# Optimization experiments

Measured on AMD Instinct MI355X. Metric: run time of the kernel, lower is better.

The kernel has to match this reference:

```python
import jax, jax.numpy as jnp
import numpy as np

B, L = 32, 100
NQ = 500
S = NQ + 1          # n_question + 1 skills
DK, DA, DE = 64, 64, 128
NE, NAT, NIT = 20000, 3000, 3000


def _xavier(k, shape):
    fan_out, fan_in = shape[0], shape[1]
    bound = float(np.sqrt(6.0 / (fan_in + fan_out)))
    return jax.random.uniform(k, shape, jnp.float32, -bound, bound)


def setup_inputs() -> dict:
    key = jax.random.key(0)
    ks = jax.random.split(key, 24)
    inp = {
        'e_data': jax.random.randint(ks[0], (B, L), 0, NE),
        'a_data': jax.random.randint(ks[1], (B, L), 0, 2, dtype=jnp.int32),
        'at_data': jax.random.randint(ks[2], (B, L), 0, NAT),
        'it_data': jax.random.randint(ks[3], (B, L), 0, NIT),
        'q_matrix': (jax.random.uniform(ks[4], (NE + 10, S)) < 0.05).astype(jnp.float32),
        'h0': _xavier(ks[5], (S, DK)),
        'e_embed': _xavier(ks[6], (NE + 10, DE)),
        'at_embed': _xavier(ks[7], (NAT + 10, DK)),
        'it_embed': _xavier(ks[8], (NIT + 10, DK)),
        'W1': _xavier(ks[9], (DK, DA + DE + DK)), 'b1': jnp.zeros((DK,)),
        'W2': _xavier(ks[10], (DK, 4 * DK)),      'b2': jnp.zeros((DK,)),
        'W3': _xavier(ks[11], (DK, 4 * DK)),      'b3': jnp.zeros((DK,)),
        'W4': _xavier(ks[12], (DK, 3 * DK)),      'b4': jnp.zeros((DK,)),
        'W5': _xavier(ks[13], (DK, DE + DK)),     'b5': jnp.zeros((DK,)),
    }
    return inp


def reference(e_data, a_data, at_data, it_data, q_matrix, h0, e_embed,
              at_embed, it_embed, W1, b1, W2, b2, W3, b3, W4, b4, W5, b5):
    b, l = e_data.shape
    dk = h0.shape[1]
    e_emb = e_embed[e_data]            # (B,L,DE)
    it_emb = it_embed[it_data]         # (B,L,DK)
    at_emb = at_embed[at_data]         # (B,L,DK)
    a_rep = jnp.broadcast_to(a_data.astype(jnp.float32)[:, :, None], (b, l, DA))
    # linear_1 over concat(e, at, a): all learning vectors, computed once
    all_learning = jnp.concatenate([e_emb, at_emb, a_rep], axis=2) @ W1.T + b1  # (B,L,DK)

    h_pre0 = jnp.broadcast_to(h0[None], (b,) + h0.shape)      # (B,S,DK)
    h_tilde0 = q_matrix[e_data[:, 0]] @ h0                    # (B,DK)
    learning0 = jnp.zeros((b, dk), jnp.float32)

    xs = dict(
        e_t=e_data[:, :-1].T,                                  # (L-1,B)
        it_t=jnp.swapaxes(it_emb[:, :-1], 0, 1),               # (L-1,B,DK)
        learn_t=jnp.swapaxes(all_learning[:, :-1], 0, 1),      # (L-1,B,DK)
        e_next=e_data[:, 1:].T,                                # (L-1,B)
        e_emb_next=jnp.swapaxes(e_emb[:, 1:], 0, 1),           # (L-1,B,DE)
    )

    def step(carry, x):
        h_pre, h_tilde_pre, learning_pre = carry
        q_e = q_matrix[x['e_t']]                               # (B,S)
        g_in = jnp.concatenate([learning_pre, x['it_t'], x['learn_t'], h_tilde_pre], 1)
        learning_gain = jnp.tanh(g_in @ W2.T + b2)
        gamma_l = jax.nn.sigmoid(g_in @ W3.T + b3)
        LG = gamma_l * (learning_gain + 1.0) * 0.5             # (B,DK)
        LG_tilde = q_e[:, :, None] * LG[:, None, :]            # (B,S,DK)
        s = h_pre.shape[1]
        f_in = jnp.concatenate([
            h_pre,
            jnp.broadcast_to(LG[:, None, :], (b, s, dk)),
            jnp.broadcast_to(x['it_t'][:, None, :], (b, s, dk)),
        ], axis=2)
        gamma_f = jax.nn.sigmoid(f_in @ W4.T + b4)             # (B,S,DK)
        h = LG_tilde + gamma_f * h_pre
        q_next = q_matrix[x['e_next']]                         # (B,S)
        h_tilde = jnp.einsum('bs,bsd->bd', q_next, h)
        y = jax.nn.sigmoid(jnp.concatenate([x['e_emb_next'], h_tilde], 1) @ W5.T + b5).sum(1) / dk
        return (h, h_tilde, x['learn_t']), y

    _, ys = jax.lax.scan(step, (h_pre0, h_tilde0, learning0), xs)
    pred = jnp.concatenate([jnp.zeros((b, 1), jnp.float32), ys.T], axis=1)  # (B,L)
    return pred
```

## Files before the change

kernel.cpp:

```cpp
#include <hip/hip_runtime.h>
#include <hip/hip_bf16.h>

namespace {

constexpr int B  = 32;
constexpr int L  = 100;
constexpr int S  = 501;
constexpr int DK = 64;
constexpr int DE = 128;

typedef __attribute__((ext_vector_type(8))) short short8v;
typedef __attribute__((ext_vector_type(4))) float f32x4;
typedef unsigned int u32;

__device__ __forceinline__ float sigm(float x) {
    return __fdividef(1.0f, 1.0f + __expf(-x));
}
__device__ __forceinline__ unsigned short f2bf(float f) {
    u32 u = __float_as_uint(f);
    u += 0x7FFFu + ((u >> 16) & 1u);
    return (unsigned short)(u >> 16);
}
__device__ __forceinline__ u32 pack2(float a, float b) {
    return (u32)f2bf(a) | ((u32)f2bf(b) << 16);
}

__global__ __launch_bounds__(256) void k_init(
    const float* __restrict__ W1, const float* __restrict__ W2,
    const float* __restrict__ W3, const float* __restrict__ W4,
    const float* __restrict__ W5,
    float* __restrict__ W1T, float* __restrict__ W2T, float* __restrict__ W3T,
    float* __restrict__ W4T, float* __restrict__ W5T,
    float* __restrict__ pred)
{
    const int idx = blockIdx.x * 256 + threadIdx.x;
    const int st  = gridDim.x * 256;
    for (int i = idx; i < 64 * 256; i += st) {
        int dd = i >> 8, kk = i & 255;
        W1T[kk * 64 + dd] = W1[i];
        W2T[kk * 64 + dd] = W2[i];
        W3T[kk * 64 + dd] = W3[i];
    }
    for (int i = idx; i < 64 * 192; i += st) {
        int dd = i / 192, kk = i % 192;
        W4T[kk * 64 + dd] = W4[i];
        W5T[kk * 64 + dd] = W5[i];
    }
    if (idx < B) pred[idx * L] = 0.0f;
}

__global__ __launch_bounds__(256) void k_all_learning(
    const int* __restrict__ e_data, const int* __restrict__ a_data,
    const int* __restrict__ at_data,
    const float* __restrict__ e_embed, const float* __restrict__ at_embed,
    const float* __restrict__ W1T, const float* __restrict__ b1,
    float* __restrict__ allL)
{
    __shared__ float in_s[4][257];
    const int g = threadIdx.x >> 6;
    const int d = threadIdx.x & 63;
    const int row = blockIdx.x * 4 + g;
    const int e  = e_data[row];
    const int at = at_data[row];
    in_s[g][d]       = e_embed[(size_t)e * DE + d];
    in_s[g][64 + d]  = e_embed[(size_t)e * DE + 64 + d];
    in_s[g][128 + d] = at_embed[(size_t)at * DK + d];
    in_s[g][192 + d] = (float)a_data[row];
    __syncthreads();
    float acc = b1[d];
    #pragma unroll 8
    for (int k = 0; k < 256; ++k) acc += W1T[k * 64 + d] * in_s[g][k];
    allL[row * DK + d] = acc;
}

__global__ __launch_bounds__(256) void k_pre(
    const int* __restrict__ e_data, const int* __restrict__ it_data,
    const float* __restrict__ e_embed, const float* __restrict__ it_embed,
    const float* __restrict__ allL,
    const float* __restrict__ W2T, const float* __restrict__ W3T,
    const float* __restrict__ W4T, const float* __restrict__ W5T,
    const float* __restrict__ b2, const float* __restrict__ b3,
    const float* __restrict__ b4, const float* __restrict__ b5,
    float* __restrict__ G2, float* __restrict__ G3,
    float* __restrict__ G4it, float* __restrict__ prey)
{
    __shared__ float lp[4][64], its[4][64], ln[4][64], ee[4][128];
    const int g = threadIdx.x >> 6;
    const int d = threadIdx.x & 63;
    const int row = blockIdx.x * 4 + g;
    const int t = row % L;
    lp[g][d]  = (t == 0) ? 0.0f : allL[(row - 1) * 64 + d];
    its[g][d] = it_embed[(size_t)it_data[row] * 64 + d];
    ln[g][d]  = allL[row * 64 + d];
    const int e = e_data[row];
    ee[g][d]      = e_embed[(size_t)e * DE + d];
    ee[g][64 + d] = e_embed[(size_t)e * DE + 64 + d];
    __syncthreads();
    float g2 = b2[d], g3 = b3[d], g4 = b4[d], py = b5[d];
    #pragma unroll 4
    for (int k = 0; k < 64; ++k) {
        const float l0 = lp[g][k], i0 = its[g][k], n0 = ln[g][k];
        g2 += W2T[k * 64 + d] * l0 + W2T[(64 + k) * 64 + d] * i0 + W2T[(128 + k) * 64 + d] * n0;
        g3 += W3T[k * 64 + d] * l0 + W3T[(64 + k) * 64 + d] * i0 + W3T[(128 + k) * 64 + d] * n0;
        g4 += W4T[(128 + k) * 64 + d] * i0;
        py += W5T[k * 64 + d] * ee[g][k] + W5T[(64 + k) * 64 + d] * ee[g][64 + k];
    }
    G2[row * 64 + d]   = g2;
    G3[row * 64 + d]   = g3;
    G4it[row * 64 + d] = g4;
    prey[row * 64 + d] = py;
}

__global__ __launch_bounds__(512, 1) void k_steps(
    const float* __restrict__ G2, const float* __restrict__ G3,
    const float* __restrict__ G4it,
    const float* __restrict__ W2, const float* __restrict__ W3,
    const float* __restrict__ W4,
    const float* __restrict__ q_matrix, const int* __restrict__ e_data,
    const float* __restrict__ h0, float* __restrict__ hthist)
{
    __shared__ unsigned short hB[512 * 72];
    __shared__ float2 qP[512];
    __shared__ float htH[100 * 64];
    __shared__ float htS[64], LGs[64], Vs[64];
    __shared__ float red[512], red2[512];
    __shared__ float red4[32 * 64];
    __shared__ int eRow[104];

    const int tid = threadIdx.x;
    const int b   = blockIdx.x;
    const int l   = tid & 63;
    const int w   = tid >> 6;
    const int lm  = l & 15;
    const int lk  = l >> 4;
    const int d   = tid & 63;
    const int kg  = tid >> 6;

    float w2r[8], w3r[8], wbr[8];
    #pragma unroll
    for (int j = 0; j < 8; ++j) {
        w2r[j] = W2[d * 256 + 192 + kg * 8 + j];
        w3r[j] = W3[d * 256 + 192 + kg * 8 + j];
        wbr[j] = W4[d * 192 + 64  + kg * 8 + j];
    }

    short8v afr[4][2];
    #pragma unroll
    for (int dt = 0; dt < 4; ++dt)
        #pragma unroll
        for (int kc = 0; kc < 2; ++kc) {
            const float* src = W4 + (size_t)(dt * 16 + lm) * 192 + kc * 32 + lk * 8;
            union { unsigned short us[8]; short8v v; } u;
            #pragma unroll
            for (int j = 0; j < 8; ++j) u.us[j] = f2bf(src[j]);
            afr[dt][kc] = u.v;
        }

    if (tid < L) eRow[tid] = e_data[b * L + tid];

    f32x4 hreg[4][4];
    #pragma unroll
    for (int st = 0; st < 4; ++st) {
        const int s = (w * 4 + st) * 16 + lm;
        #pragma unroll
        for (int dt = 0; dt < 4; ++dt) {
            const int d0 = dt * 16 + lk * 4;
            f32x4 hv = {0.f, 0.f, 0.f, 0.f};
            if (s < S) hv = *(const f32x4*)(h0 + (size_t)s * 64 + d0);
            hreg[st][dt] = hv;
            *(uint2*)&hB[s * 72 + d0] =
                make_uint2(pack2(hv.x, hv.y), pack2(hv.z, hv.w));
        }
    }
    __syncthreads();

    {
        const float q0 = (tid < S) ? q_matrix[(size_t)eRow[0] * S + tid] : 0.f;
        const float q1 = (tid < S) ? q_matrix[(size_t)eRow[1] * S + tid] : 0.f;
        qP[tid] = make_float2(q0, q1);
    }
    float g2v = 0.f, g3v = 0.f, g4v = 0.f;
    if (tid < 64) {
        g2v = G2[(b * L) * 64 + l];
        g3v = G3[(b * L) * 64 + l];
        g4v = G4it[(b * L) * 64 + l];
    }
    __syncthreads();

    {
        f32x4 part[4];
        #pragma unroll
        for (int dt = 0; dt < 4; ++dt) part[dt] = f32x4{0.f, 0.f, 0.f, 0.f};
        #pragma unroll
        for (int st = 0; st < 4; ++st) {
            const int s = (w * 4 + st) * 16 + lm;
            const float qe = qP[s].x;
            #pragma unroll
            for (int dt = 0; dt < 4; ++dt) part[dt] += qe * hreg[st][dt];
        }
        #pragma unroll
        for (int dt = 0; dt < 4; ++dt)
            #pragma unroll
            for (int i = 0; i < 4; ++i) {
                float v = part[dt][i];
                v += __shfl_xor(v, 1); v += __shfl_xor(v, 2);
                part[dt][i] = v;
            }
        if ((lm & 3) == 0) {
            const int g = w * 4 + (lm >> 2);
            #pragma unroll
            for (int dt = 0; dt < 4; ++dt)
                *(f32x4*)&red4[g * 64 + dt * 16 + lk * 4] = part[dt];
        }
    }
    __syncthreads();
    if (tid < 64) {
        float htd = 0.f;
        #pragma unroll
        for (int g = 0; g < 32; ++g) htd += red4[g * 64 + l];
        htS[l] = htd;
        htH[l] = htd;
    }
    __syncthreads();

    float qn_reg = 0.f;

    for (int t = 0; t < L - 1; ++t) {
        if (t > 0) {
            const float2 qold = qP[tid];
            qP[tid] = make_float2(qold.y, qn_reg);
        }
        {
            const int tn = (t + 2 < L) ? t + 2 : L - 1;
            qn_reg = (tid < S) ? q_matrix[(size_t)eRow[tn] * S + tid] : 0.f;
        }
        short8v bfr[4][2];
        #pragma unroll
        for (int st = 0; st < 4; ++st) {
            const int s = (w * 4 + st) * 16 + lm;
            #pragma unroll
            for (int kc = 0; kc < 2; ++kc)
                bfr[st][kc] = *(const short8v*)&hB[s * 72 + kc * 32 + lk * 8];
        }
        {
            const f32x4 h4a = *(const f32x4*)&htS[kg * 8];
            const f32x4 h4b = *(const f32x4*)&htS[kg * 8 + 4];
            float p2 = 0.f, p3 = 0.f;
            #pragma unroll
            for (int j = 0; j < 4; ++j) {
                p2 += w2r[j] * h4a[j] + w2r[4 + j] * h4b[j];
                p3 += w3r[j] * h4a[j] + w3r[4 + j] * h4b[j];
            }
            red[kg * 64 + d]  = p2;
            red2[kg * 64 + d] = p3;
        }
        __syncthreads();

        if (tid < 64) {
            float g2 = g2v, g3 = g3v;
            #pragma unroll
            for (int ww = 0; ww < 8; ++ww) { g2 += red[ww * 64 + d]; g3 += red2[ww * 64 + d]; }
            LGs[d] = sigm(g3) * (tanhf(g2) + 1.0f) * 0.5f;
        }
        __syncthreads();

        {
            const f32x4 l4a = *(const f32x4*)&LGs[kg * 8];
            const f32x4 l4b = *(const f32x4*)&LGs[kg * 8 + 4];
            float pv = 0.f;
            #pragma unroll
            for (int j = 0; j < 4; ++j)
                pv += wbr[j] * l4a[j] + wbr[4 + j] * l4b[j];
            red[kg * 64 + d] = pv;
        }
        __syncthreads();

        if (tid < 64) {
            float v = g4v;
            #pragma unroll
            for (int ww = 0; ww < 8; ++ww) v += red[ww * 64 + d];
            Vs[d] = v;
            g2v = G2[(b * L + t + 1) * 64 + l];
            g3v = G3[(b * L + t + 1) * 64 + l];
            g4v = G4it[(b * L + t + 1) * 64 + l];
        }
        __syncthreads();

        float2 qv[4];
        #pragma unroll
        for (int st = 0; st < 4; ++st) qv[st] = qP[(w * 4 + st) * 16 + lm];

        f32x4 part[4];
        #pragma unroll
        for (int dt = 0; dt < 4; ++dt) part[dt] = f32x4{0.f, 0.f, 0.f, 0.f};

        #pragma unroll
        for (int half = 0; half < 2; ++half) {
            f32x4 acc[2][4];
            #pragma unroll
            for (int d2 = 0; d2 < 2; ++d2)
                #pragma unroll
                for (int st = 0; st < 4; ++st) acc[d2][st] = f32x4{0.f, 0.f, 0.f, 0.f};

            #pragma unroll
            for (int d2 = 0; d2 < 2; ++d2) {
                const int dt = half * 2 + d2;
                #pragma unroll
                for (int st = 0; st < 4; ++st) {
                    acc[d2][st] = __builtin_amdgcn_mfma_f32_16x16x32_bf16(
                        afr[dt][0], bfr[st][0], acc[d2][st], 0, 0, 0);
                    acc[d2][st] = __builtin_amdgcn_mfma_f32_16x16x32_bf16(
                        afr[dt][1], bfr[st][1], acc[d2][st], 0, 0, 0);
                }
            }

            #pragma unroll
            for (int d2 = 0; d2 < 2; ++d2) {
                const int dt = half * 2 + d2;
                const int d0 = dt * 16 + lk * 4;
                const f32x4 lg4 = *(const f32x4*)&LGs[d0];
                const f32x4 v4  = *(const f32x4*)&Vs[d0];
                #pragma unroll
                for (int st = 0; st < 4; ++st) {
                    const int s = (w * 4 + st) * 16 + lm;
                    const float qe = qv[st].x;
                    const float qq = qv[st].y;
                    const f32x4 a  = acc[d2][st];
                    const f32x4 ho = hreg[st][dt];
                    f32x4 hn;
                    hn.x = qe * lg4.x + sigm(a.x + v4.x) * ho.x;
                    hn.y = qe * lg4.y + sigm(a.y + v4.y) * ho.y;
                    hn.z = qe * lg4.z + sigm(a.z + v4.z) * ho.z;
                    hn.w = qe * lg4.w + sigm(a.w + v4.w) * ho.w;
                    hreg[st][dt] = hn;
                    *(uint2*)&hB[s * 72 + d0] =
                        make_uint2(pack2(hn.x, hn.y), pack2(hn.z, hn.w));
                    part[dt] += qq * hn;
                }
            }
        }

        #pragma unroll
        for (int dt = 0; dt < 4; ++dt)
            #pragma unroll
            for (int i = 0; i < 4; ++i) {
                float v = part[dt][i];
                v += __shfl_xor(v, 1); v += __shfl_xor(v, 2);
                part[dt][i] = v;
            }
        if ((lm & 3) == 0) {
            const int g = w * 4 + (lm >> 2);
            #pragma unroll
            for (int dt = 0; dt < 4; ++dt)
                *(f32x4*)&red4[g * 64 + dt * 16 + lk * 4] = part[dt];
        }
        __syncthreads();

        if (tid < 64) {
            float htd = 0.f;
            #pragma unroll
            for (int g = 0; g < 32; ++g) htd += red4[g * 64 + l];
            htS[l] = htd;
            htH[(t + 1) * 64 + l] = htd;
        }
        __syncthreads();
    }

    for (int i = tid; i < 100 * 64; i += 512)
        hthist[(size_t)(i >> 6) * (B * 64) + b * 64 + (i & 63)] = htH[i];
}

__global__ __launch_bounds__(64) void k_y(
    const float* __restrict__ hthist, const float* __restrict__ prey,
    const float* __restrict__ W5T, float* __restrict__ pred)
{
    __shared__ float HT[64];
    const int j = blockIdx.x + 1;
    const int b = blockIdx.y;
    const int d = threadIdx.x;
    HT[d] = hthist[(size_t)j * (B * 64) + b * 64 + d];
    __syncthreads();
    float acc = prey[(b * L + j) * 64 + d];
    #pragma unroll 8
    for (int k = 0; k < 64; ++k) acc += W5T[(128 + k) * 64 + d] * HT[k];
    float y = sigm(acc);
    #pragma unroll
    for (int m = 1; m < 64; m <<= 1) y += __shfl_xor(y, m);
    if (d == 0) pred[b * L + j] = y * (1.0f / 64.0f);
}

}

extern "C" void kernel_launch(void* const* d_in, const int* in_sizes, int n_in,
                              void* d_out, int out_size, void* d_ws, size_t ws_size,
                              hipStream_t stream)
{
    const int*   e_data   = (const int*)d_in[0];
    const int*   a_data   = (const int*)d_in[1];
    const int*   at_data  = (const int*)d_in[2];
    const int*   it_data  = (const int*)d_in[3];
    const float* q_matrix = (const float*)d_in[4];
    const float* h0       = (const float*)d_in[5];
    const float* e_embed  = (const float*)d_in[6];
    const float* at_embed = (const float*)d_in[7];
    const float* it_embed = (const float*)d_in[8];
    const float* W1 = (const float*)d_in[9];  const float* b1 = (const float*)d_in[10];
    const float* W2 = (const float*)d_in[11]; const float* b2 = (const float*)d_in[12];
    const float* W3 = (const float*)d_in[13]; const float* b3 = (const float*)d_in[14];
    const float* W4 = (const float*)d_in[15]; const float* b4 = (const float*)d_in[16];
    const float* W5 = (const float*)d_in[17]; const float* b5 = (const float*)d_in[18];
    float* pred = (float*)d_out;

    float* ws   = (float*)d_ws;
    float* W1T    = ws;
    float* W2T    = W1T    + 16384;
    float* W3T    = W2T    + 16384;
    float* W4T    = W3T    + 16384;
    float* W5T    = W4T    + 12288;
    float* allL   = W5T    + 12288;
    float* G2     = allL   + 204800;
    float* G3     = G2     + 204800;
    float* G4it   = G3     + 204800;
    float* prey   = G4it   + 204800;
    float* hthist = prey   + 204800;

    hipLaunchKernelGGL(k_init, dim3(64), dim3(256), 0, stream,
                       W1, W2, W3, W4, W5, W1T, W2T, W3T, W4T, W5T, pred);
    hipLaunchKernelGGL(k_all_learning, dim3(B * L / 4), dim3(256), 0, stream,
                       e_data, a_data, at_data, e_embed, at_embed, W1T, b1, allL);
    hipLaunchKernelGGL(k_pre, dim3(B * L / 4), dim3(256), 0, stream,
                       e_data, it_data, e_embed, it_embed, allL,
                       W2T, W3T, W4T, W5T, b2, b3, b4, b5, G2, G3, G4it, prey);
    hipLaunchKernelGGL(k_steps, dim3(B), dim3(512), 0, stream,
                       G2, G3, G4it, W2, W3, W4, q_matrix, e_data, h0, hthist);
    hipLaunchKernelGGL(k_y, dim3(L - 1, B), dim3(64), 0, stream,
                       hthist, prey, W5T, pred);
}
```

Before: 755.1 us.

## Move forget-gate MFMA off the critical path and pad reduction buffer

The per-step h_pre·W4 MFMA product depends only on the previous h, so it is now computed right after h is updated and stored, rather than after the gate-vector reduction and barrier of the next step. This lets the matrix work overlap with the small vector phase, at the cost of keeping a full 4x4 accumulator array in registers across iterations. The red4 reduction buffer is padded to a stride of 68 to reduce LDS bank conflicts, and the ht reduction is moved to the loop head. pack2 now rounds to bf16 by adding half an ulp instead of round-to-nearest-even, which saves a few integer ops per value but changes tie rounding slightly.

Result: faster. 726.4 us (median of 2 runs) (-3.8%).

```diff
diff --git a/kernel.cpp b/kernel.cpp
--- a/kernel.cpp
+++ b/kernel.cpp
@@ -22,7 +22,9 @@
     return (unsigned short)(u >> 16);
 }
 __device__ __forceinline__ u32 pack2(float a, float b) {
-    return (u32)f2bf(a) | ((u32)f2bf(b) << 16);
+    const u32 ua = __float_as_uint(a) + 0x8000u;
+    const u32 ub = __float_as_uint(b) + 0x8000u;
+    return (ua >> 16) | (ub & 0xFFFF0000u);
 }
 
 __global__ __launch_bounds__(256) void k_init(
@@ -124,7 +126,7 @@
     __shared__ float htH[100 * 64];
     __shared__ float htS[64], LGs[64], Vs[64];
     __shared__ float red[512], red2[512];
-    __shared__ float red4[32 * 64];
+    __shared__ float red4[32 * 68];
     __shared__ int eRow[104];
 
     const int tid = threadIdx.x;
@@ -172,6 +174,27 @@
                 make_uint2(pack2(hv.x, hv.y), pack2(hv.z, hv.w));
         }
     }
+
+    f32x4 acc[4][4];
+    {
+        short8v bfr[4][2];
+        #pragma unroll
+        for (int st = 0; st < 4; ++st) {
+            const int s = (w * 4 + st) * 16 + lm;
+            #pragma unroll
+            for (int kc = 0; kc < 2; ++kc)
+                bfr[st][kc] = *(const short8v*)&hB[s * 72 + kc * 32 + lk * 8];
+        }
+        #pragma unroll
+        for (int dt = 0; dt < 4; ++dt)
+            #pragma unroll
+            for (int st = 0; st < 4; ++st) {
+                f32x4 z = {0.f, 0.f, 0.f, 0.f};
+                z = __builtin_amdgcn_mfma_f32_16x16x32_bf16(afr[dt][0], bfr[st][0], z, 0, 0, 0);
+                z = __builtin_amdgcn_mfma_f32_16x16x32_bf16(afr[dt][1], bfr[st][1], z, 0, 0, 0);
+                acc[dt][st] = z;
+            }
+    }
     __syncthreads();
 
     {
@@ -210,22 +233,23 @@
             const int g = w * 4 + (lm >> 2);
             #pragma unroll
             for (int dt = 0; dt < 4; ++dt)
-                *(f32x4*)&red4[g * 64 + dt * 16 + lk * 4] = part[dt];
-        }
-    }
-    __syncthreads();
-    if (tid < 64) {
-        float htd = 0.f;
-        #pragma unroll
-        for (int g = 0; g < 32; ++g) htd += red4[g * 64 + l];
-        htS[l] = htd;
-        htH[l] = htd;
+                *(f32x4*)&red4[g * 68 + dt * 16 + lk * 4] = part[dt];
+        }
     }
     __syncthreads();
 
     float qn_reg = 0.f;
 
     for (int t = 0; t < L - 1; ++t) {
+        if (tid < 64) {
+            float htd = 0.f;
+            #pragma unroll
+            for (int g = 0; g < 32; ++g) htd += red4[g * 68 + l];
+            htS[l] = htd;
+            htH[t * 64 + l] = htd;
+        }
+        __syncthreads();
+
         if (t > 0) {
             const float2 qold = qP[tid];
             qP[tid] = make_float2(qold.y, qn_reg);
@@ -233,14 +257,6 @@
         {
             const int tn = (t + 2 < L) ? t + 2 : L - 1;
             qn_reg = (tid < S) ? q_matrix[(size_t)eRow[tn] * S + tid] : 0.f;
-        }
-        short8v bfr[4][2];
-        #pragma unroll
-        for (int st = 0; st < 4; ++st) {
-            const int s = (w * 4 + st) * 16 + lm;
-            #pragma unroll
-            for (int kc = 0; kc < 2; ++kc)
-                bfr[st][kc] = *(const short8v*)&hB[s * 72 + kc * 32 + lk * 8];
         }
         {
             const f32x4 h4a = *(const f32x4*)&htS[kg * 8];
@@ -295,49 +311,47 @@
         for (int dt = 0; dt < 4; ++dt) part[dt] = f32x4{0.f, 0.f, 0.f, 0.f};
 
         #pragma unroll
-        for (int half = 0; half < 2; ++half) {
-            f32x4 acc[2][4];
-            #pragma unroll
-            for (int d2 = 0; d2 < 2; ++d2)
+        for (int dt = 0; dt < 4; ++dt) {
+            const int d0 = dt * 16 + lk * 4;
+            const f32x4 lg4 = *(const f32x4*)&LGs[d0];
+            const f32x4 v4  = *(const f32x4*)&Vs[d0];
+            #pragma unroll
+            for (int st = 0; st < 4; ++st) {
+                const int s = (w * 4 + st) * 16 + lm;
+                const float qe = qv[st].x;
+                const float qq = qv[st].y;
+                const f32x4 a  = acc[dt][st];
+                const f32x4 ho = hreg[st][dt];
+                f32x4 hn;
+                hn.x = qe * lg4.x + sigm(a.x + v4.x) * ho.x;
+                hn.y = qe * lg4.y + sigm(a.y + v4.y) * ho.y;
+                hn.z = qe * lg4.z + sigm(a.z + v4.z) * ho.z;
+                hn.w = qe * lg4.w + sigm(a.w + v4.w) * ho.w;
+                hreg[st][dt] = hn;
+                *(uint2*)&hB[s * 72 + d0] =
+                    make_uint2(pack2(hn.x, hn.y), pack2(hn.z, hn.w));
+                part[dt] += qq * hn;
+            }
+        }
+
+        if (t < L - 2) {
+            short8v bfr[4][2];
+            #pragma unroll
+            for (int st = 0; st < 4; ++st) {
+                const int s = (w * 4 + st) * 16 + lm;
                 #pragma unroll
-                for (int st = 0; st < 4; ++st) acc[d2][st] = f32x4{0.f, 0.f, 0.f, 0.f};
-
-            #pragma unroll
-            for (int d2 = 0; d2 < 2; ++d2) {
-                const int dt = half * 2 + d2;
+                for (int kc = 0; kc < 2; ++kc)
+                    bfr[st][kc] = *(const short8v*)&hB[s * 72 + kc * 32 + lk * 8];
+            }
+            #pragma unroll
+            for (int dt = 0; dt < 4; ++dt)
                 #pragma unroll
                 for (int st = 0; st < 4; ++st) {
-                    acc[d2][st] = __builtin_amdgcn_mfma_f32_16x16x32_bf16(
-                        afr[dt][0], bfr[st][0], acc[d2][st], 0, 0, 0);
-                    acc[d2][st] = __builtin_amdgcn_mfma_f32_16x16x32_bf16(
-                        afr[dt][1], bfr[st][1], acc[d2][st], 0, 0, 0);
+                    f32x4 z = {0.f, 0.f, 0.f, 0.f};
+                    z = __builtin_amdgcn_mfma_f32_16x16x32_bf16(afr[dt][0], bfr[st][0], z, 0, 0, 0);
+                    z = __builtin_amdgcn_mfma_f32_16x16x32_bf16(afr[dt][1], bfr[st][1], z, 0, 0, 0);
+                    acc[dt][st] = z;
                 }
-            }
-
-            #pragma unroll
-            for (int d2 = 0; d2 < 2; ++d2) {
-                const int dt = half * 2 + d2;
-                const int d0 = dt * 16 + lk * 4;
-                const f32x4 lg4 = *(const f32x4*)&LGs[d0];
-                const f32x4 v4  = *(const f32x4*)&Vs[d0];
-                #pragma unroll
-                for (int st = 0; st < 4; ++st) {
-                    const int s = (w * 4 + st) * 16 + lm;
-                    const float qe = qv[st].x;
-                    const float qq = qv[st].y;
-                    const f32x4 a  = acc[d2][st];
-                    const f32x4 ho = hreg[st][dt];
-                    f32x4 hn;
-                    hn.x = qe * lg4.x + sigm(a.x + v4.x) * ho.x;
-                    hn.y = qe * lg4.y + sigm(a.y + v4.y) * ho.y;
-                    hn.z = qe * lg4.z + sigm(a.z + v4.z) * ho.z;
-                    hn.w = qe * lg4.w + sigm(a.w + v4.w) * ho.w;
-                    hreg[st][dt] = hn;
-                    *(uint2*)&hB[s * 72 + d0] =
-                        make_uint2(pack2(hn.x, hn.y), pack2(hn.z, hn.w));
-                    part[dt] += qq * hn;
-                }
-            }
         }
 
         #pragma unroll
@@ -352,20 +366,18 @@
             const int g = w * 4 + (lm >> 2);
             #pragma unroll
             for (int dt = 0; dt < 4; ++dt)
-                *(f32x4*)&red4[g * 64 + dt * 16 + lk * 4] = part[dt];
-        }
-        __syncthreads();
-
-        if (tid < 64) {
-            float htd = 0.f;
-            #pragma unroll
-            for (int g = 0; g < 32; ++g) htd += red4[g * 64 + l];
-            htS[l] = htd;
-            htH[(t + 1) * 64 + l] = htd;
-        }
-        __syncthreads();
-    }
-
+                *(f32x4*)&red4[g * 68 + dt * 16 + lk * 4] = part[dt];
+        }
+        __syncthreads();
+    }
+
+    if (tid < 64) {
+        float htd = 0.f;
+        #pragma unroll
+        for (int g = 0; g < 32; ++g) htd += red4[g * 68 + l];
+        htH[99 * 64 + l] = htd;
+    }
+    __syncthreads();
     for (int i = tid; i < 100 * 64; i += 512)
         hthist[(size_t)(i >> 6) * (B * 64) + b * 64 + (i & 63)] = htH[i];
 }
```
